# Kernel tuning notes

Hardware: AMD Instinct MI355X
Metric: run time of the kernel (lower is better)

Reference implementation:

```python
import jax, jax.numpy as jnp
import numpy as np

HEADS = 4
CH = 64  # hidden_channels (per-head out channels)
N_INT = 50000
N_LANE = 400000
E_PO = 400000
E_ADJ = 200000


def setup_inputs() -> dict:
    key = jax.random.key(0)
    ks = iter(jax.random.split(key, 32))
    rn = lambda shape, s=0.1: jax.random.normal(next(ks), shape, dtype=jnp.float32) * s
    inp = {
        'x_int': rn((N_INT, 16), 1.0),
        'x_lane': rn((N_LANE, 12), 1.0),
        'h0': jnp.zeros((N_INT, CH), jnp.float32),
        'enc_int_W': rn((16, CH)), 'enc_int_b': jnp.zeros((CH,), jnp.float32),
        'enc_lane_W': rn((12, CH)), 'enc_lane_b': jnp.zeros((CH,), jnp.float32),
        'Wsrc_po': rn((CH, HEADS * CH)), 'Wdst_po': rn((CH, HEADS * CH)),
        'att_src_po': rn((HEADS, CH)), 'att_dst_po': rn((HEADS, CH)),
        'bias_po': jnp.zeros((HEADS * CH,), jnp.float32),
        'Wsrc_adj': rn((CH, HEADS * CH)), 'Wdst_adj': rn((CH, HEADS * CH)),
        'att_src_adj': rn((HEADS, CH)), 'att_dst_adj': rn((HEADS, CH)),
        'bias_adj': jnp.zeros((HEADS * CH,), jnp.float32),
        'gru_W_ih': rn((3 * CH, HEADS * CH)), 'gru_W_hh': rn((3 * CH, CH)),
        'gru_b_ih': jnp.zeros((3 * CH,), jnp.float32), 'gru_b_hh': jnp.zeros((3 * CH,), jnp.float32),
        'W_pi': rn((CH, 8)), 'b_pi': jnp.zeros((8,), jnp.float32),
        'W_v': rn((CH, 1)), 'b_v': jnp.zeros((1,), jnp.float32),
        'src_po': jax.random.randint(next(ks), (E_PO,), 0, N_LANE),
        'dst_po': jax.random.randint(next(ks), (E_PO,), 0, N_INT),
        'src_adj': jax.random.randint(next(ks), (E_ADJ,), 0, N_INT),
        'dst_adj': jax.random.randint(next(ks), (E_ADJ,), 0, N_INT),
    }
    return inp


def gat_conv(x_src, x_dst, src, dst, Wsrc, Wdst, a_src, a_dst, bias, n_dst):
    # PyG GATConv (bipartite, concat=True, no self loops), negative_slope=0.2
    hs = (x_src @ Wsrc).reshape(-1, HEADS, CH)  # [Ns,H,C]
    hd = (x_dst @ Wdst).reshape(-1, HEADS, CH)  # [Nd,H,C]
    a_s = jnp.einsum('nhc,hc->nh', hs, a_src)   # [Ns,H]
    a_d = jnp.einsum('nhc,hc->nh', hd, a_dst)   # [Nd,H]
    alpha = jax.nn.leaky_relu(a_s[src] + a_d[dst], 0.2)        # [E,H]
    amax = jax.ops.segment_max(alpha, dst, num_segments=n_dst)  # [Nd,H]
    ex = jnp.exp(alpha - amax[dst])
    den = jax.ops.segment_sum(ex, dst, num_segments=n_dst)
    w = ex / den[dst]                                           # [E,H] softmax per dst
    msg = hs[src] * w[:, :, None]                               # [E,H,C]
    out = jax.ops.segment_sum(msg, dst, num_segments=n_dst)     # [Nd,H,C]
    return out.reshape(n_dst, HEADS * CH) + bias


def gru_cell(x, h, W_ih, W_hh, b_ih, b_hh):
    gi = x @ W_ih.T + b_ih
    gh = h @ W_hh.T + b_hh
    i_r, i_z, i_n = jnp.split(gi, 3, axis=1)
    h_r, h_z, h_n = jnp.split(gh, 3, axis=1)
    r = jax.nn.sigmoid(i_r + h_r)
    z = jax.nn.sigmoid(i_z + h_z)
    n = jnp.tanh(i_n + r * h_n)
    return (1.0 - z) * n + z * h


def reference(x_int, x_lane, h0, enc_int_W, enc_int_b, enc_lane_W, enc_lane_b,
              Wsrc_po, Wdst_po, att_src_po, att_dst_po, bias_po,
              Wsrc_adj, Wdst_adj, att_src_adj, att_dst_adj, bias_adj,
              gru_W_ih, gru_W_hh, gru_b_ih, gru_b_hh,
              W_pi, b_pi, W_v, b_v,
              src_po, dst_po, src_adj, dst_adj):
    # per-type encoders + ReLU
    e_int = jax.nn.relu(x_int @ enc_int_W + enc_int_b)    # [N_int,CH]
    e_lane = jax.nn.relu(x_lane @ enc_lane_W + enc_lane_b)  # [N_lane,CH]
    # HeteroConv aggr='sum' over relations targeting 'intersection'
    o_po = gat_conv(e_lane, e_int, src_po, dst_po, Wsrc_po, Wdst_po,
                    att_src_po, att_dst_po, bias_po, N_INT)
    o_adj = gat_conv(e_int, e_int, src_adj, dst_adj, Wsrc_adj, Wdst_adj,
                     att_src_adj, att_dst_adj, bias_adj, N_INT)
    inter = jax.nn.relu(o_po + o_adj)  # dropout = identity (deterministic eval)
    h_new = gru_cell(inter, h0, gru_W_ih, gru_W_hh, gru_b_ih, gru_b_hh)
    logits = h_new @ W_pi + b_pi
    value = h_new @ W_v + b_v
    return logits, value, h_new
```

## Files before the change

kernel.cpp:

```cpp
#include <hip/hip_runtime.h>

#define NI 50000
#define NL 400000
#define EPO 400000
#define EADJ 200000

#define K1_ITER 8
#define K2_ITER 4
#define K1_ROWS (32*K1_ITER)
#define K2_ROWS (32*K2_ITER)
#define NLB ((NL + K1_ROWS - 1)/K1_ROWS)
#define NIB ((NI + K2_ROWS - 1)/K2_ROWS)
#define NHB ((EPO + EADJ + 255)/256)

typedef unsigned int u32;
typedef unsigned short u16;
typedef short bf16x8 __attribute__((ext_vector_type(8)));
typedef float f32x4 __attribute__((ext_vector_type(4)));

__device__ __forceinline__ float bf2f(u16 h){ return __uint_as_float(((u32)h)<<16); }
__device__ __forceinline__ u16 f2bf(float f){
  u32 u = __float_as_uint(f);
  u += 0x7FFFu + ((u>>16)&1u);
  return (u16)(u>>16);
}
__device__ __forceinline__ u32 pack2(float a, float b){
  return (u32)f2bf(a) | ((u32)f2bf(b)<<16);
}

__device__ __forceinline__ float b2_val(
    const float* __restrict__ W_ih, const float* __restrict__ W_hh, int m, int k)
{
  if(k < 256){ return (m<192) ? W_ih[m*256+k] : 0.f; }
  int kk = k-256;
  if(m<128) return W_hh[m*64+kk];
  if(m>=192) return W_hh[(m-64)*64+kk];
  return 0.f;
}

__global__ __launch_bounds__(256) void k0_prep(
    const float* __restrict__ Wsrc_po, const float* __restrict__ att_src_po,
    const float* __restrict__ Wdst_po, const float* __restrict__ att_dst_po,
    const float* __restrict__ Wsrc_adj, const float* __restrict__ att_src_adj,
    const float* __restrict__ Wdst_adj, const float* __restrict__ att_dst_adj,
    const float* __restrict__ W_ih, const float* __restrict__ W_hh,
    const float* __restrict__ bias_po, const float* __restrict__ bias_adj,
    const float* __restrict__ b_ih, const float* __restrict__ b_hh,
    float* __restrict__ v4, u16* __restrict__ WheadF, u16* __restrict__ B2F,
    float* __restrict__ bias_comb, float* __restrict__ bias2,
    int* __restrict__ cnt)
{
  const int T0 = 1024, T1 = 4*4*4*64*8, T2 = 10*16*64*8;
  const int TC = 2*NI;
  int total = T0 + T1 + T2 + 256 + 256 + TC;
  for(int t = blockIdx.x*256 + threadIdx.x; t < total; t += gridDim.x*256){
    if(t < T0){
      int which = t>>8, hc = t&255, h = hc>>6, c = hc&63;
      const float *W, *att;
      if(which==0){ W=Wsrc_po;  att=att_src_po; }
      else if(which==1){ W=Wdst_po;  att=att_dst_po; }
      else if(which==2){ W=Wsrc_adj; att=att_src_adj; }
      else { W=Wdst_adj; att=att_dst_adj; }
      float s=0.f;
      for(int j=0;j<64;j++) s += W[c*256 + h*64 + j]*att[h*64+j];
      v4[which*256 + hc] = s;
    } else if(t < T0 + T1){
      int i = t - T0;
      int j = i&7;
      int u4 = i>>3;
      int lane = u4&63;
      int rem = u4>>6;
      int ct = rem&3, kt = (rem>>2)&3, h = rem>>4;
      int r = lane&15, qb = lane>>4;
      int kp = kt*32 + qb*8 + j;
      int n = ct*16 + r;
      float val = (kp<64) ? Wsrc_po[kp*256 + h*64 + n]
                          : Wsrc_adj[(kp-64)*256 + h*64 + n];
      WheadF[i] = f2bf(val);
    } else if(t < T0 + T1 + T2){
      int i = t - (T0+T1);
      int j = i&7;
      int u4 = i>>3;
      int kstep = u4>>10, rem = u4&1023, tile = rem>>6, lane = rem&63;
      int col = tile*16 + (lane&15);
      int k = kstep*32 + (lane>>4)*8 + j;
      B2F[i] = f2bf(b2_val(W_ih, W_hh, col, k));
    } else if(t < T0 + T1 + T2 + 256){
      int m = t - (T0+T1+T2);
      bias_comb[m] = bias_po[m] + bias_adj[m];
    } else if(t < T0 + T1 + T2 + 512){
      int m = t - (T0+T1+T2+256);
      float v;
      if(m<128) v = b_ih[m] + b_hh[m];
      else if(m<192) v = b_ih[m];
      else v = b_hh[m-64];
      bias2[m] = v;
    } else {
      cnt[t - (T0+T1+T2+512)] = 0;
    }
  }
}

__global__ __launch_bounds__(256) void k_enc(
    const float* __restrict__ x_lane, const float* __restrict__ Wl, const float* __restrict__ bl,
    const float* __restrict__ x_int,  const float* __restrict__ Wi, const float* __restrict__ bi,
    const float* __restrict__ v_sp, const float* __restrict__ v_dp,
    const float* __restrict__ v_sa, const float* __restrict__ v_da,
    u16* __restrict__ e_lane, float* __restrict__ a_s_po,
    u16* __restrict__ e_int, float* __restrict__ a_dp, float* __restrict__ a_sa,
    float* __restrict__ a_da,
    const int* __restrict__ dst_po, const int* __restrict__ dst_adj,
    int* __restrict__ cnt)
{
  int t = threadIdx.x;
  int wv = t>>6, l = t&63;
  int g = l&7, m = l>>3;
  int blk = blockIdx.x;
  if(blk < NLB){
    float wreg[12][8], breg[8];
#pragma unroll
    for(int k=0;k<12;k++){
      float4 w0 = *(const float4*)(Wl + k*64 + g*8);
      float4 w1 = *(const float4*)(Wl + k*64 + g*8 + 4);
      wreg[k][0]=w0.x; wreg[k][1]=w0.y; wreg[k][2]=w0.z; wreg[k][3]=w0.w;
      wreg[k][4]=w1.x; wreg[k][5]=w1.y; wreg[k][6]=w1.z; wreg[k][7]=w1.w;
    }
    {
      float4 b0 = *(const float4*)(bl + g*8);
      float4 b1 = *(const float4*)(bl + g*8 + 4);
      breg[0]=b0.x; breg[1]=b0.y; breg[2]=b0.z; breg[3]=b0.w;
      breg[4]=b1.x; breg[5]=b1.y; breg[6]=b1.z; breg[7]=b1.w;
    }
    int rowbase = blk*K1_ROWS + wv*(8*K1_ITER) + m;
    float4 Aa={0,0,0,0}, Ab={0,0,0,0}, Ac={0,0,0,0};
    float4 Ba={0,0,0,0}, Bb={0,0,0,0}, Bc={0,0,0,0};
    if(rowbase < NL){
      const float4* xp = (const float4*)(x_lane + (size_t)rowbase*12);
      Aa = xp[0]; Ab = xp[1]; Ac = xp[2];
    }
    if(rowbase+8 < NL){
      const float4* xp = (const float4*)(x_lane + (size_t)(rowbase+8)*12);
      Ba = xp[0]; Bb = xp[1]; Bc = xp[2];
    }
#pragma unroll
    for(int it=0; it<K1_ITER; it++){
      int row = rowbase + it*8;
      float4 Ca={0,0,0,0}, Cb={0,0,0,0}, Cc={0,0,0,0};
      if(it+2 < K1_ITER && row+16 < NL){
        const float4* xp = (const float4*)(x_lane + (size_t)(row+16)*12);
        Ca = xp[0]; Cb = xp[1]; Cc = xp[2];
      }
      float xv[12];
      xv[0]=Aa.x; xv[1]=Aa.y; xv[2]=Aa.z; xv[3]=Aa.w;
      xv[4]=Ab.x; xv[5]=Ab.y; xv[6]=Ab.z; xv[7]=Ab.w;
      xv[8]=Ac.x; xv[9]=Ac.y; xv[10]=Ac.z; xv[11]=Ac.w;
      float acc[8];
#pragma unroll
      for(int j=0;j<8;j++) acc[j]=breg[j];
#pragma unroll
      for(int k=0;k<12;k++){
        float xk = xv[k];
#pragma unroll
        for(int j=0;j<8;j++) acc[j] += xk*wreg[k][j];
      }
      float e[8];
#pragma unroll
      for(int j=0;j<8;j++) e[j] = fmaxf(acc[j], 0.f);
      float as[4];
#pragma unroll
      for(int h=0;h<4;h++){
        float4 v0 = *(const float4*)(v_sp + h*64 + g*8);
        float4 v1 = *(const float4*)(v_sp + h*64 + g*8 + 4);
        as[h] = e[0]*v0.x + e[1]*v0.y + e[2]*v0.z + e[3]*v0.w
              + e[4]*v1.x + e[5]*v1.y + e[6]*v1.z + e[7]*v1.w;
      }
#pragma unroll
      for(int o=1;o<8;o<<=1){
#pragma unroll
        for(int h=0;h<4;h++) as[h] += __shfl_xor(as[h], o, 64);
      }
      if(row < NL){
        uint4 P;
        P.x = pack2(e[0],e[1]); P.y = pack2(e[2],e[3]);
        P.z = pack2(e[4],e[5]); P.w = pack2(e[6],e[7]);
        ((uint4*)e_lane)[(size_t)row*8 + g] = P;
        if(g==0){
          float4 A; A.x=as[0]; A.y=as[1]; A.z=as[2]; A.w=as[3];
          *(float4*)(a_s_po + (size_t)row*4) = A;
        }
      }
      Aa=Ba; Ab=Bb; Ac=Bc;
      Ba=Ca; Bb=Cb; Bc=Cc;
    }
  } else if(blk < NLB + NIB){
    int b2 = blk - NLB;
    float breg[8];
    {
      float4 b0 = *(const float4*)(bi + g*8);
      float4 b1 = *(const float4*)(bi + g*8 + 4);
      breg[0]=b0.x; breg[1]=b0.y; breg[2]=b0.z; breg[3]=b0.w;
      breg[4]=b1.x; breg[5]=b1.y; breg[6]=b1.z; breg[7]=b1.w;
    }
    int rowbase = b2*K2_ROWS + wv*(8*K2_ITER) + m;
#pragma unroll
    for(int it=0; it<K2_ITER; it++){
      int row = rowbase + it*8;
      float xv[16];
      if(row < NI){
        const float4* xp = (const float4*)(x_int + (size_t)row*16);
#pragma unroll
        for(int q=0;q<4;q++){
          float4 xq = xp[q];
          xv[q*4]=xq.x; xv[q*4+1]=xq.y; xv[q*4+2]=xq.z; xv[q*4+3]=xq.w;
        }
      } else {
#pragma unroll
        for(int k=0;k<16;k++) xv[k]=0.f;
      }
      float acc[8];
#pragma unroll
      for(int j=0;j<8;j++) acc[j]=breg[j];
#pragma unroll
      for(int k=0;k<16;k++){
        float4 w0 = *(const float4*)(Wi + k*64 + g*8);
        float4 w1 = *(const float4*)(Wi + k*64 + g*8 + 4);
        float xk = xv[k];
        acc[0] += xk*w0.x; acc[1] += xk*w0.y; acc[2] += xk*w0.z; acc[3] += xk*w0.w;
        acc[4] += xk*w1.x; acc[5] += xk*w1.y; acc[6] += xk*w1.z; acc[7] += xk*w1.w;
      }
      float e[8];
#pragma unroll
      for(int j=0;j<8;j++) e[j] = fmaxf(acc[j], 0.f);
      float ad[4], sa[4], da[4];
#pragma unroll
      for(int h=0;h<4;h++){
        float4 v0, v1;
        v0 = *(const float4*)(v_dp + h*64 + g*8); v1 = *(const float4*)(v_dp + h*64 + g*8 + 4);
        ad[h] = e[0]*v0.x + e[1]*v0.y + e[2]*v0.z + e[3]*v0.w
              + e[4]*v1.x + e[5]*v1.y + e[6]*v1.z + e[7]*v1.w;
        v0 = *(const float4*)(v_sa + h*64 + g*8); v1 = *(const float4*)(v_sa + h*64 + g*8 + 4);
        sa[h] = e[0]*v0.x + e[1]*v0.y + e[2]*v0.z + e[3]*v0.w
              + e[4]*v1.x + e[5]*v1.y + e[6]*v1.z + e[7]*v1.w;
        v0 = *(const float4*)(v_da + h*64 + g*8); v1 = *(const float4*)(v_da + h*64 + g*8 + 4);
        da[h] = e[0]*v0.x + e[1]*v0.y + e[2]*v0.z + e[3]*v0.w
              + e[4]*v1.x + e[5]*v1.y + e[6]*v1.z + e[7]*v1.w;
      }
#pragma unroll
      for(int o=1;o<8;o<<=1){
#pragma unroll
        for(int h=0;h<4;h++){
          ad[h] += __shfl_xor(ad[h], o, 64);
          sa[h] += __shfl_xor(sa[h], o, 64);
          da[h] += __shfl_xor(da[h], o, 64);
        }
      }
      if(row < NI){
        uint4 P;
        P.x = pack2(e[0],e[1]); P.y = pack2(e[2],e[3]);
        P.z = pack2(e[4],e[5]); P.w = pack2(e[6],e[7]);
        ((uint4*)e_int)[(size_t)row*8 + g] = P;
        if(g==0){
          float4 A;
          A.x=ad[0]; A.y=ad[1]; A.z=ad[2]; A.w=ad[3]; *(float4*)(a_dp + (size_t)row*4) = A;
          A.x=sa[0]; A.y=sa[1]; A.z=sa[2]; A.w=sa[3]; *(float4*)(a_sa + (size_t)row*4) = A;
          A.x=da[0]; A.y=da[1]; A.z=da[2]; A.w=da[3]; *(float4*)(a_da + (size_t)row*4) = A;
        }
      }
    }
  } else {
    int i = (blk - NLB - NIB)*256 + t;
    if(i < EPO) atomicAdd(&cnt[dst_po[i]], 1);
    else if(i < EPO+EADJ) atomicAdd(&cnt[NI + dst_adj[i-EPO]], 1);
  }
}

__global__ __launch_bounds__(1024) void k4a_scan(
    const int* __restrict__ cnt, int* __restrict__ offA, int* __restrict__ bsum)
{
  __shared__ int s[1024];
  int y = blockIdx.y;
  int i = blockIdx.x*1024 + threadIdx.x;
  int v = (i<NI) ? cnt[y*NI+i] : 0;
  s[threadIdx.x]=v;
  __syncthreads();
  for(int o=1;o<1024;o<<=1){
    int t = (threadIdx.x>=o) ? s[threadIdx.x-o] : 0;
    __syncthreads();
    s[threadIdx.x] += t;
    __syncthreads();
  }
  if(i<NI) offA[y*NI+i] = s[threadIdx.x]-v;
  if(threadIdx.x==1023) bsum[y*64+blockIdx.x] = s[1023];
}

__global__ __launch_bounds__(128) void k4b_scanb(int* __restrict__ bsum)
{
  int y = threadIdx.x>>6, lane = threadIdx.x&63;
  int v = (lane<49) ? bsum[y*64+lane] : 0;
  int orig = v;
#pragma unroll
  for(int o=1;o<64;o<<=1){
    int t = __shfl_up(v,o,64);
    if(lane>=o) v += t;
  }
  if(lane<49) bsum[y*64+lane] = v-orig;
}

__global__ __launch_bounds__(1024) void k4c_add(
    int* __restrict__ offA, int* __restrict__ cur, const int* __restrict__ bsum)
{
  int y = blockIdx.y;
  int i = blockIdx.x*1024 + threadIdx.x;
  if(i<NI){
    int o = offA[y*NI+i] + bsum[y*64+blockIdx.x];
    offA[y*NI+i]=o;
    cur[y*NI+i]=o;
  }
}

__global__ __launch_bounds__(256) void k5_scatter(
    const int* __restrict__ src_po, const int* __restrict__ dst_po,
    const int* __restrict__ src_adj, const int* __restrict__ dst_adj,
    const float* __restrict__ a_s_po, const float* __restrict__ a_d_po,
    const float* __restrict__ a_s_adj, const float* __restrict__ a_d_adj,
    int* __restrict__ cur, int* __restrict__ csr_po, int* __restrict__ csr_adj,
    float* __restrict__ pw_po, float* __restrict__ pw_adj)
{
  int i = blockIdx.x*256 + threadIdx.x;
  if(i < EPO){
    int s = src_po[i];
    int d = dst_po[i];
    int p = atomicAdd(&cur[d],1);
    csr_po[p] = s;
    float4 as = *(const float4*)(a_s_po + (size_t)s*4);
    float4 ad = *(const float4*)(a_d_po + (size_t)d*4);
    float4 pv;
    float x;
    x = as.x+ad.x; pv.x = __expf(x>0.f?x:0.2f*x);
    x = as.y+ad.y; pv.y = __expf(x>0.f?x:0.2f*x);
    x = as.z+ad.z; pv.z = __expf(x>0.f?x:0.2f*x);
    x = as.w+ad.w; pv.w = __expf(x>0.f?x:0.2f*x);
    *(float4*)(pw_po + (size_t)p*4) = pv;
  } else if(i < EPO+EADJ){
    int e = i-EPO;
    int s = src_adj[e];
    int d = dst_adj[e];
    int p = atomicAdd(&cur[NI+d],1);
    csr_adj[p] = s;
    float4 as = *(const float4*)(a_s_adj + (size_t)s*4);
    float4 ad = *(const float4*)(a_d_adj + (size_t)d*4);
    float4 pv;
    float x;
    x = as.x+ad.x; pv.x = __expf(x>0.f?x:0.2f*x);
    x = as.y+ad.y; pv.y = __expf(x>0.f?x:0.2f*x);
    x = as.z+ad.z; pv.z = __expf(x>0.f?x:0.2f*x);
    x = as.w+ad.w; pv.w = __expf(x>0.f?x:0.2f*x);
    *(float4*)(pw_adj + (size_t)p*4) = pv;
  }
}

__device__ __forceinline__ void agg_rel(
    int beg, int n, int lane,
    const int* __restrict__ csr, const float* __restrict__ pw,
    const u16* __restrict__ emat, u16* __restrict__ aggrow)
{
  float l0=0,l1=0,l2=0,l3=0;
  float c0=0,c1=0,c2=0,c3=0;
  for(int base=0;base<n;base+=64){
    int m = n-base; if(m>64) m=64;
    int sv_ = (lane<m) ? csr[beg+base+lane] : 0;
    int t2=0;
    for(; t2+3<m; t2+=4){
      int s0 = __shfl(sv_, t2,   64);
      int s1 = __shfl(sv_, t2+1, 64);
      int s2 = __shfl(sv_, t2+2, 64);
      int s3 = __shfl(sv_, t2+3, 64);
      float4 p0 = *(const float4*)(pw + (size_t)(beg+base+t2  )*4);
      float4 p1 = *(const float4*)(pw + (size_t)(beg+base+t2+1)*4);
      float4 p2 = *(const float4*)(pw + (size_t)(beg+base+t2+2)*4);
      float4 p3 = *(const float4*)(pw + (size_t)(beg+base+t2+3)*4);
      float e0 = bf2f(emat[(size_t)s0*64+lane]);
      float e1 = bf2f(emat[(size_t)s1*64+lane]);
      float e2 = bf2f(emat[(size_t)s2*64+lane]);
      float e3 = bf2f(emat[(size_t)s3*64+lane]);
      c0 += p0.x*e0; c1 += p0.y*e0; c2 += p0.z*e0; c3 += p0.w*e0;
      l0 += p0.x;    l1 += p0.y;    l2 += p0.z;    l3 += p0.w;
      c0 += p1.x*e1; c1 += p1.y*e1; c2 += p1.z*e1; c3 += p1.w*e1;
      l0 += p1.x;    l1 += p1.y;    l2 += p1.z;    l3 += p1.w;
      c0 += p2.x*e2; c1 += p2.y*e2; c2 += p2.z*e2; c3 += p2.w*e2;
      l0 += p2.x;    l1 += p2.y;    l2 += p2.z;    l3 += p2.w;
      c0 += p3.x*e3; c1 += p3.y*e3; c2 += p3.z*e3; c3 += p3.w*e3;
      l0 += p3.x;    l1 += p3.y;    l2 += p3.z;    l3 += p3.w;
    }
    for(; t2<m; t2++){
      int s0 = __shfl(sv_, t2, 64);
      float4 p0 = *(const float4*)(pw + (size_t)(beg+base+t2)*4);
      float e0 = bf2f(emat[(size_t)s0*64+lane]);
      c0 += p0.x*e0; c1 += p0.y*e0; c2 += p0.z*e0; c3 += p0.w*e0;
      l0 += p0.x;    l1 += p0.y;    l2 += p0.z;    l3 += p0.w;
    }
  }
  aggrow[lane]       = f2bf(n>0 ? c0/l0 : 0.f);
  aggrow[64+lane]    = f2bf(n>0 ? c1/l1 : 0.f);
  aggrow[128+lane]   = f2bf(n>0 ? c2/l2 : 0.f);
  aggrow[192+lane]   = f2bf(n>0 ? c3/l3 : 0.f);
}

__global__ __launch_bounds__(512) void k6_agg(
    const int* __restrict__ off, const int* __restrict__ cnt,
    const int* __restrict__ csr_po, const int* __restrict__ csr_adj,
    const float* __restrict__ pw_po, const float* __restrict__ pw_adj,
    const u16* __restrict__ e_lane, const u16* __restrict__ e_int,
    u16* __restrict__ agg)
{
  int wave=threadIdx.x>>6, lane=threadIdx.x&63;
  int d = blockIdx.x*4 + (wave&3);
  if(d>=NI) return;
  if(wave < 4)
    agg_rel(off[d],    cnt[d],    lane, csr_po,  pw_po,  e_lane, agg + (size_t)d*512);
  else
    agg_rel(off[NI+d], cnt[NI+d], lane, csr_adj, pw_adj, e_int,  agg + (size_t)d*512 + 256);
}

__global__ __launch_bounds__(256) void k8_fused(
    const u16* __restrict__ agg, const uint4* __restrict__ WheadF,
    const float* __restrict__ bias_comb,
    const uint4* __restrict__ B2F, const float* __restrict__ bias2,
    const float* __restrict__ h0,
    const float* __restrict__ Wpi, const float* __restrict__ bpi,
    const float* __restrict__ Wv, const float* __restrict__ bvp,
    float* __restrict__ out)
{
  __shared__ u16 interT[64][264];
  int t=threadIdx.x, w=t>>6, lane=t&63;
  int r = lane&15, q = lane>>4;
  int row0 = blockIdx.x*64;
  int h = w;

  const uint4* BF = WheadF + (size_t)h*16*64;
#pragma unroll
  for(int rt=0; rt<4; rt++){
    int row = row0 + rt*16 + r;
    int arc = row < NI ? row : NI-1;
    const u16* arow_p = agg + (size_t)arc*512;
    bf16x8 af[4];
#pragma unroll
    for(int kt=0; kt<4; kt++){
      int colbase = (kt<2) ? (h*64 + kt*32) : (256 + h*64 + (kt-2)*32);
      af[kt] = *(const bf16x8*)(arow_p + colbase + q*8);
    }
#pragma unroll
    for(int ct=0; ct<4; ct++){
      f32x4 facc = {0,0,0,0};
#pragma unroll
      for(int kt=0; kt<4; kt++){
        uint4 bu = BF[(kt*4 + ct)*64 + lane];
        bf16x8 bfr; *(uint4*)&bfr = bu;
        facc = __builtin_amdgcn_mfma_f32_16x16x32_bf16(af[kt], bfr, facc, 0,0,0);
      }
      int col = h*64 + ct*16 + r;
      float bcol = bias_comb[col];
#pragma unroll
      for(int rr=0; rr<4; rr++)
        interT[rt*16 + q*4 + rr][col] = f2bf(fmaxf(facc[rr]+bcol, 0.f));
    }
  }
  __syncthreads();

  int arowl = w*16 + r;
  int arow  = row0 + arowl;
  int arc = arow < NI ? arow : NI-1;
  const float* h0r = h0 + (size_t)arc*64 + q*8;
  f32x4 acc[16];
#pragma unroll
  for(int i=0;i<16;i++) acc[i] = (f32x4){0,0,0,0};
#pragma unroll
  for(int ks=0; ks<10; ks++){
    bf16x8 af;
    if(ks < 8){
      af = *(const bf16x8*)&interT[arowl][ks*32 + q*8];
    } else {
      const float* hp = h0r + (ks-8)*32;
      float4 f0 = *(const float4*)(hp);
      float4 f1 = *(const float4*)(hp+4);
      uint4 P;
      P.x = pack2(f0.x,f0.y); P.y = pack2(f0.z,f0.w);
      P.z = pack2(f1.x,f1.y); P.w = pack2(f1.z,f1.w);
      *(uint4*)&af = P;
    }
    const uint4* bp = B2F + ks*1024 + lane;
#pragma unroll
    for(int tt=0;tt<16;tt++){
      uint4 bu = bp[tt*64];
      bf16x8 bfr; *(uint4*)&bfr = bu;
      acc[tt] = __builtin_amdgcn_mfma_f32_16x16x32_bf16(af, bfr, acc[tt], 0,0,0);
    }
  }
  float pk[4][8];
  float pv[4];
#pragma unroll
  for(int rr=0;rr<4;rr++){
    pv[rr]=0.f;
#pragma unroll
    for(int j=0;j<8;j++) pk[rr][j]=0.f;
  }
  int rbase = row0 + w*16 + q*4;
#pragma unroll
  for(int t2=0;t2<4;t2++){
    int c = t2*16 + r;
    float b0 = bias2[c], b1 = bias2[64+c], b2 = bias2[128+c], b3 = bias2[192+c];
    float wp[8];
#pragma unroll
    for(int j=0;j<8;j++) wp[j] = Wpi[c*8+j];
    float wv = Wv[c];
#pragma unroll
    for(int rr=0;rr<4;rr++){
      int row = rbase + rr;
      float g0 = acc[t2][rr]    + b0;
      float g1 = acc[t2+4][rr]  + b1;
      float g2 = acc[t2+8][rr]  + b2;
      float g3 = acc[t2+12][rr] + b3;
      float h0v = (row < NI) ? h0[(size_t)row*64 + c] : 0.f;
      float rg = 1.f/(1.f+__expf(-g0));
      float zg = 1.f/(1.f+__expf(-g1));
      float e2 = __expf(2.f*(g2 + rg*g3));
      float ng = 1.f - 2.f/(e2+1.f);
      float hh = (1.f-zg)*ng + zg*h0v;
      if(row < NI) out[450000 + (size_t)row*64 + c] = hh;
#pragma unroll
      for(int j=0;j<8;j++) pk[rr][j] += hh*wp[j];
      pv[rr] += hh*wv;
    }
  }
#pragma unroll
  for(int o=1;o<16;o<<=1){
#pragma unroll
    for(int rr=0;rr<4;rr++){
#pragma unroll
      for(int j=0;j<8;j++) pk[rr][j] += __shfl_xor(pk[rr][j], o, 64);
      pv[rr] += __shfl_xor(pv[rr], o, 64);
    }
  }
  if(r==0){
#pragma unroll
    for(int rr=0;rr<4;rr++){
      int row = rbase + rr;
      if(row < NI){
#pragma unroll
        for(int j=0;j<8;j++) out[(size_t)row*8 + j] = pk[rr][j] + bpi[j];
        out[400000 + row] = pv[rr] + bvp[0];
      }
    }
  }
}

extern "C" void kernel_launch(void* const* d_in, const int* in_sizes, int n_in,
                              void* d_out, int out_size, void* d_ws, size_t ws_size,
                              hipStream_t stream) {
  const float* x_int      = (const float*)d_in[0];
  const float* x_lane     = (const float*)d_in[1];
  const float* h0         = (const float*)d_in[2];
  const float* enc_int_W  = (const float*)d_in[3];
  const float* enc_int_b  = (const float*)d_in[4];
  const float* enc_lane_W = (const float*)d_in[5];
  const float* enc_lane_b = (const float*)d_in[6];
  const float* Wsrc_po    = (const float*)d_in[7];
  const float* Wdst_po    = (const float*)d_in[8];
  const float* att_src_po = (const float*)d_in[9];
  const float* att_dst_po = (const float*)d_in[10];
  const float* bias_po    = (const float*)d_in[11];
  const float* Wsrc_adj   = (const float*)d_in[12];
  const float* Wdst_adj   = (const float*)d_in[13];
  const float* att_src_adj= (const float*)d_in[14];
  const float* att_dst_adj= (const float*)d_in[15];
  const float* bias_adj   = (const float*)d_in[16];
  const float* gru_W_ih   = (const float*)d_in[17];
  const float* gru_W_hh   = (const float*)d_in[18];
  const float* gru_b_ih   = (const float*)d_in[19];
  const float* gru_b_hh   = (const float*)d_in[20];
  const float* W_pi       = (const float*)d_in[21];
  const float* b_pi       = (const float*)d_in[22];
  const float* W_v        = (const float*)d_in[23];
  const float* b_v        = (const float*)d_in[24];
  const int* src_po  = (const int*)d_in[25];
  const int* dst_po  = (const int*)d_in[26];
  const int* src_adj = (const int*)d_in[27];
  const int* dst_adj = (const int*)d_in[28];
  float* out = (float*)d_out;

  char* w = (char*)d_ws;
  size_t ofs = 0;
  auto alloc = [&](size_t bytes)->char*{
    char* p = w + ofs;
    ofs = (ofs + bytes + 255) & ~(size_t)255;
    return p;
  };
  u16*  e_lane   = (u16*)alloc((size_t)NL*64*2);
  u16*  e_int    = (u16*)alloc((size_t)NI*64*2);
  float* a_s_po  = (float*)alloc((size_t)NL*4*4);
  float* a_d_po  = (float*)alloc((size_t)NI*4*4);
  float* a_s_adj = (float*)alloc((size_t)NI*4*4);
  float* a_d_adj = (float*)alloc((size_t)NI*4*4);
  int*  cnt      = (int*)alloc((size_t)2*NI*4);
  int*  offA     = (int*)alloc((size_t)2*NI*4);
  int*  cur      = (int*)alloc((size_t)2*NI*4);
  int*  csr_po   = (int*)alloc((size_t)EPO*4);
  int*  csr_adj  = (int*)alloc((size_t)EADJ*4);
  float* pw_po   = (float*)alloc((size_t)EPO*4*4);
  float* pw_adj  = (float*)alloc((size_t)EADJ*4*4);
  int*  bsum     = (int*)alloc(2*64*4);
  u16*  agg      = (u16*)alloc((size_t)NI*512*2);
  u16*  WheadF   = (u16*)alloc(4*4*4*64*8*2);
  u16*  B2F      = (u16*)alloc(10*16*64*8*2);
  float* v4      = (float*)alloc(4*256*4);
  float* bias_comb = (float*)alloc(256*4);
  float* bias2   = (float*)alloc(256*4);
  (void)ws_size; (void)n_in; (void)in_sizes; (void)out_size;

  k0_prep<<<256, 256, 0, stream>>>(
      Wsrc_po, att_src_po, Wdst_po, att_dst_po,
      Wsrc_adj, att_src_adj, Wdst_adj, att_dst_adj,
      gru_W_ih, gru_W_hh, bias_po, bias_adj, gru_b_ih, gru_b_hh,
      v4, WheadF, B2F, bias_comb, bias2, cnt);
  k_enc<<<NLB+NIB+NHB, 256, 0, stream>>>(
      x_lane, enc_lane_W, enc_lane_b,
      x_int, enc_int_W, enc_int_b,
      v4 + 0, v4 + 256, v4 + 512, v4 + 768,
      e_lane, a_s_po, e_int, a_d_po, a_s_adj, a_d_adj,
      dst_po, dst_adj, cnt);
  k4a_scan<<<dim3(49,2), 1024, 0, stream>>>(cnt, offA, bsum);
  k4b_scanb<<<1, 128, 0, stream>>>(bsum);
  k4c_add<<<dim3(49,2), 1024, 0, stream>>>(offA, cur, bsum);
  k5_scatter<<<(EPO+EADJ+255)/256, 256, 0, stream>>>(src_po, dst_po, src_adj, dst_adj,
      a_s_po, a_d_po, a_s_adj, a_d_adj,
      cur, csr_po, csr_adj, pw_po, pw_adj);
  k6_agg<<<(NI+3)/4, 512, 0, stream>>>(offA, cnt, csr_po, csr_adj,
      pw_po, pw_adj, e_lane, e_int, agg);
  k8_fused<<<(NI+63)/64, 256, 0, stream>>>(agg, (const uint4*)WheadF, bias_comb,
      (const uint4*)B2F, bias2, h0, W_pi, b_pi, W_v, b_v, out);
}
```

Baseline: 404.7 us.

## Replace three-kernel scan with atomic-cursor single pass; stage agg tiles in LDS

The three-kernel exclusive scan (block scan, block-sum scan, add) becomes one kernel. Each wave scans 256 counts with shuffles and claims its base offset from a global cursor with an atomicAdd, which removes two launches. The resulting offsets are no longer in node order, but each segment stays contiguous, so CSR consumers that use off and cnt per node still work. k8_fused now loops over heads and loads agg rows into shared memory with coalesced uint4 loads before the MFMA fragments are read, at the cost of extra syncthreads and LDS.

```diff
diff --git a/kernel.cpp b/kernel.cpp
--- a/kernel.cpp
+++ b/kernel.cpp
@@ -48,11 +48,11 @@
     const float* __restrict__ b_ih, const float* __restrict__ b_hh,
     float* __restrict__ v4, u16* __restrict__ WheadF, u16* __restrict__ B2F,
     float* __restrict__ bias_comb, float* __restrict__ bias2,
-    int* __restrict__ cnt)
+    int* __restrict__ cnt, int* __restrict__ cursor)
 {
   const int T0 = 1024, T1 = 4*4*4*64*8, T2 = 10*16*64*8;
   const int TC = 2*NI;
-  int total = T0 + T1 + T2 + 256 + 256 + TC;
+  int total = T0 + T1 + T2 + 256 + 256 + TC + 2;
   for(int t = blockIdx.x*256 + threadIdx.x; t < total; t += gridDim.x*256){
     if(t < T0){
       int which = t>>8, hc = t&255, h = hc>>6, c = hc&63;
@@ -95,8 +95,10 @@
       else if(m<192) v = b_ih[m];
       else v = b_hh[m-64];
       bias2[m] = v;
+    } else if(t < T0 + T1 + T2 + 512 + TC){
+      cnt[t - (T0+T1+T2+512)] = 0;
     } else {
-      cnt[t - (T0+T1+T2+512)] = 0;
+      cursor[t - (T0+T1+T2+512+TC)] = 0;
     }
   }
 }
@@ -274,47 +276,44 @@
   }
 }
 
-__global__ __launch_bounds__(1024) void k4a_scan(
-    const int* __restrict__ cnt, int* __restrict__ offA, int* __restrict__ bsum)
-{
-  __shared__ int s[1024];
+__global__ __launch_bounds__(256) void k4_scan(
+    const int* __restrict__ cnt, int* __restrict__ offA, int* __restrict__ cur,
+    int* __restrict__ cursor)
+{
   int y = blockIdx.y;
-  int i = blockIdx.x*1024 + threadIdx.x;
-  int v = (i<NI) ? cnt[y*NI+i] : 0;
-  s[threadIdx.x]=v;
-  __syncthreads();
-  for(int o=1;o<1024;o<<=1){
-    int t = (threadIdx.x>=o) ? s[threadIdx.x-o] : 0;
-    __syncthreads();
-    s[threadIdx.x] += t;
-    __syncthreads();
-  }
-  if(i<NI) offA[y*NI+i] = s[threadIdx.x]-v;
-  if(threadIdx.x==1023) bsum[y*64+blockIdx.x] = s[1023];
-}
-
-__global__ __launch_bounds__(128) void k4b_scanb(int* __restrict__ bsum)
-{
-  int y = threadIdx.x>>6, lane = threadIdx.x&63;
-  int v = (lane<49) ? bsum[y*64+lane] : 0;
-  int orig = v;
-#pragma unroll
-  for(int o=1;o<64;o<<=1){
-    int t = __shfl_up(v,o,64);
-    if(lane>=o) v += t;
-  }
-  if(lane<49) bsum[y*64+lane] = v-orig;
-}
-
-__global__ __launch_bounds__(1024) void k4c_add(
-    int* __restrict__ offA, int* __restrict__ cur, const int* __restrict__ bsum)
-{
-  int y = blockIdx.y;
-  int i = blockIdx.x*1024 + threadIdx.x;
-  if(i<NI){
-    int o = offA[y*NI+i] + bsum[y*64+blockIdx.x];
-    offA[y*NI+i]=o;
-    cur[y*NI+i]=o;
+  int wid = threadIdx.x>>6, lane = threadIdx.x&63;
+  int base_i = (blockIdx.x*4 + wid)*256;
+  int v[4], inc[4], ctot[4];
+#pragma unroll
+  for(int c=0;c<4;c++){
+    int i = base_i + c*64 + lane;
+    v[c] = (i<NI) ? cnt[(size_t)y*NI+i] : 0;
+    int x = v[c];
+#pragma unroll
+    for(int o=1;o<64;o<<=1){
+      int tt = __shfl_up(x,o,64);
+      if(lane>=o) x += tt;
+    }
+    inc[c] = x;
+    ctot[c] = __shfl(x, 63, 64);
+  }
+  int cpre[4];
+  cpre[0]=0;
+  cpre[1]=ctot[0];
+  cpre[2]=cpre[1]+ctot[1];
+  cpre[3]=cpre[2]+ctot[2];
+  int wtot = cpre[3]+ctot[3];
+  int base = 0;
+  if(lane==0) base = atomicAdd(&cursor[y], wtot);
+  base = __shfl(base, 0, 64);
+#pragma unroll
+  for(int c=0;c<4;c++){
+    int i = base_i + c*64 + lane;
+    if(i<NI){
+      int o = base + cpre[c] + inc[c] - v[c];
+      offA[(size_t)y*NI+i] = o;
+      cur[(size_t)y*NI+i]  = o;
+    }
   }
 }
 
@@ -431,24 +430,29 @@
     const float* __restrict__ Wv, const float* __restrict__ bvp,
     float* __restrict__ out)
 {
+  __shared__ u16 As[64][136];
   __shared__ u16 interT[64][264];
   int t=threadIdx.x, w=t>>6, lane=t&63;
   int r = lane&15, q = lane>>4;
   int row0 = blockIdx.x*64;
-  int h = w;
-
-  const uint4* BF = WheadF + (size_t)h*16*64;
-#pragma unroll
-  for(int rt=0; rt<4; rt++){
-    int row = row0 + rt*16 + r;
-    int arc = row < NI ? row : NI-1;
-    const u16* arow_p = agg + (size_t)arc*512;
+
+  for(int h=0;h<4;h++){
+#pragma unroll
+    for(int it=0; it<4; it++){
+      int lrow = it*4 + q;
+      int grow = row0 + w*16 + lrow;
+      int arc = grow < NI ? grow : NI-1;
+      int u4p = lane&15;
+      int co = (u4p<8) ? (h*64 + u4p*8) : (256 + h*64 + (u4p-8)*8);
+      uint4 v = *(const uint4*)(agg + (size_t)arc*512 + co);
+      *(uint4*)&As[w*16 + lrow][u4p*8] = v;
+    }
+    __syncthreads();
     bf16x8 af[4];
 #pragma unroll
-    for(int kt=0; kt<4; kt++){
-      int colbase = (kt<2) ? (h*64 + kt*32) : (256 + h*64 + (kt-2)*32);
-      af[kt] = *(const bf16x8*)(arow_p + colbase + q*8);
-    }
+    for(int kt=0;kt<4;kt++)
+      af[kt] = *(const bf16x8*)&As[w*16 + r][q*8 + kt*32];
+    const uint4* BF = WheadF + (size_t)h*16*64;
 #pragma unroll
     for(int ct=0; ct<4; ct++){
       f32x4 facc = {0,0,0,0};
@@ -462,7 +466,7 @@
       float bcol = bias_comb[col];
 #pragma unroll
       for(int rr=0; rr<4; rr++)
-        interT[rt*16 + q*4 + rr][col] = f2bf(fmaxf(facc[rr]+bcol, 0.f));
+        interT[w*16 + q*4 + rr][col] = f2bf(fmaxf(facc[rr]+bcol, 0.f));
     }
   }
   __syncthreads();
@@ -608,7 +612,7 @@
   int*  csr_adj  = (int*)alloc((size_t)EADJ*4);
   float* pw_po   = (float*)alloc((size_t)EPO*4*4);
   float* pw_adj  = (float*)alloc((size_t)EADJ*4*4);
-  int*  bsum     = (int*)alloc(2*64*4);
+  int*  cursor   = (int*)alloc(2*4);
   u16*  agg      = (u16*)alloc((size_t)NI*512*2);
   u16*  WheadF   = (u16*)alloc(4*4*4*64*8*2);
   u16*  B2F      = (u16*)alloc(10*16*64*8*2);
@@ -621,16 +625,14 @@
       Wsrc_po, att_src_po, Wdst_po, att_dst_po,
       Wsrc_adj, att_src_adj, Wdst_adj, att_dst_adj,
       gru_W_ih, gru_W_hh, bias_po, bias_adj, gru_b_ih, gru_b_hh,
-      v4, WheadF, B2F, bias_comb, bias2, cnt);
+      v4, WheadF, B2F, bias_comb, bias2, cnt, cursor);
   k_enc<<<NLB+NIB+NHB, 256, 0, stream>>>(
       x_lane, enc_lane_W, enc_lane_b,
       x_int, enc_int_W, enc_int_b,
       v4 + 0, v4 + 256, v4 + 512, v4 + 768,
       e_lane, a_s_po, e_int, a_d_po, a_s_adj, a_d_adj,
       dst_po, dst_adj, cnt);
-  k4a_scan<<<dim3(49,2), 1024, 0, stream>>>(cnt, offA, bsum);
-  k4b_scanb<<<1, 128, 0, stream>>>(bsum);
-  k4c_add<<<dim3(49,2), 1024, 0, stream>>>(offA, cur, bsum);
+  k4_scan<<<dim3((NI+1023)/1024, 2), 256, 0, stream>>>(cnt, offA, cur, cursor);
   k5_scatter<<<(EPO+EADJ+255)/256, 256, 0, stream>>>(src_po, dst_po, src_adj, dst_adj,
       a_s_po, a_d_po, a_s_adj, a_d_adj,
       cur, csr_po, csr_adj, pw_po, pw_adj);
```

Result: faster. 354.5 us (-12.4%).
